# Kernel optimization log

Measured on AMD Instinct MI355X. Metric: run time of the kernel, lower is better.

The kernel has to match this reference:

```python
import jax, jax.numpy as jnp
import numpy as np

N, E, G = 20000, 320000, 128
H, TE, CD = 128, 128, 64
HEADS, DH = 4, 32          # inner = 128 == H
L = 6


def _fwd(p, edge_index, batch):
    """Faithful forward of CrystalDiffusionModel (eval mode: dropout = identity).
    EquivariantGraphConv (imported in the original) is implemented as the standard
    edge-conditioned message-passing conv: m_ij = silu(W[h_src; h_dst; e_ij] + b),
    agg = scatter_add over dst, h' = W_u[h; agg] + b_u."""
    x, ea, t = p['x'], p['edge_attr'], p['t']
    n = x.shape[0]
    h = x @ p['Wn'] + p['bn']                      # [N,H] node embedding
    ef = ea @ p['We'] + p['be']                    # [E,H] edge embedding

    # sinusoidal time embedding -> MLP
    half = TE // 2
    freq = jnp.exp(-jnp.arange(half, dtype=jnp.float32) * (np.log(10000.0) / (half - 1)))
    te = t[:, None] * freq[None, :]
    te = jnp.concatenate([jnp.sin(te), jnp.cos(te)], axis=-1)          # [G,TE]
    te = jax.nn.silu(te @ p['tm_W1'] + p['tm_b1']) @ p['tm_W2'] + p['tm_b2']

    def mlp2(z, W1, b1, W2, b2):
        return jax.nn.silu(z @ W1 + b1) @ W2 + b2

    topo_e = mlp2(p['topo_cond'], p['topo_W1'], p['topo_b1'], p['topo_W2'], p['topo_b2'])
    stab_e = mlp2(p['stab_cond'], p['stab_W1'], p['stab_b1'], p['stab_W2'], p['stab_b2'])
    sust_e = mlp2(p['sust_cond'], p['sust_W1'], p['sust_b1'], p['sust_W2'], p['sust_b2'])
    cond = mlp2(jnp.concatenate([topo_e, stab_e, sust_e], axis=-1),
                p['comb_W1'], p['comb_b1'], p['comb_W2'], p['comb_b2'])  # [G,CD]

    ctx = cond[batch]                               # [N,CD] per-node condition
    # context is a single token per query -> k,v constant across layers
    k = (ctx @ p['Wk']).reshape(n, HEADS, DH)
    v = (ctx @ p['Wv']).reshape(n, HEADS, DH)
    ti = jax.nn.silu(te)[batch]                     # [N,H] time influence (dropout=id)

    src, dst = edge_index[0], edge_index[1]
    scale = DH ** -0.5
    for i in range(L):
        Wm, bm = p['gnn_Wm'][i], p['gnn_bm'][i]
        # split concat-GEMM to avoid materializing [E, 3H]
        m = jax.nn.silu(h[src] @ Wm[:H] + h[dst] @ Wm[H:2 * H] + ef @ Wm[2 * H:] + bm)
        agg = jax.ops.segment_sum(m, dst, num_segments=n)               # [N,H]
        Wu, bu = p['gnn_Wu'][i], p['gnn_bu'][i]
        hu = h @ Wu[:H] + agg @ Wu[H:] + bu
        # LayerNorm
        mu = hu.mean(-1, keepdims=True)
        var = hu.var(-1, keepdims=True)
        hu = (hu - mu) * jax.lax.rsqrt(var + 1e-5) * p['ln_g'][i] + p['ln_b'][i]
        # cross-attention; context length is 1 so softmax over j is exactly 1
        q = (hu @ p['Wq']).reshape(n, HEADS, DH)
        sim = jnp.einsum('nhd,nhd->nh', q, k) * scale                   # [N,heads]
        attn = jax.nn.softmax(sim[..., None], axis=-1)                  # == 1.0
        out = (attn * v).reshape(n, HEADS * DH)
        hu = out @ p['Wo'] + p['bo']
        h = h + hu + ti                              # residual + time influence

    node_pred = jax.nn.silu(h @ p['np_W1'] + p['np_b1']) @ p['np_W2'] + p['np_b2']
    pos_pred = jax.nn.silu(h @ p['pp_W1'] + p['pp_b1']) @ p['pp_W2'] + p['pp_b2']
    return node_pred, pos_pred


def setup_inputs() -> dict:
    key = jax.random.key(0)
    it = iter(jax.random.split(key, 96))

    def nrm(shape, s=0.02):
        return jax.random.normal(next(it), shape, jnp.float32) * s

    z = lambda *s: jnp.zeros(s, jnp.float32)
    inp = {
        'x': jax.random.normal(next(it), (N, 12), jnp.float32),
        'edge_index': jax.random.randint(next(it), (2, E), 0, N),
        'edge_attr': jax.random.normal(next(it), (E, 20), jnp.float32),
        'pos': jax.random.normal(next(it), (N, 3), jnp.float32),
        't': jax.random.uniform(next(it), (G,), jnp.float32) * 1000.0,
        'topo_cond': jax.random.normal(next(it), (G, 7), jnp.float32),
        'stab_cond': jax.random.normal(next(it), (G, 2), jnp.float32),
        'sust_cond': jax.random.normal(next(it), (G, 3), jnp.float32),
        'batch': jnp.sort(jax.random.randint(next(it), (N,), 0, G)),
        'Wn': nrm((12, H)), 'bn': z(H), 'We': nrm((20, H)), 'be': z(H),
        'tm_W1': nrm((TE, 2 * TE)), 'tm_b1': z(2 * TE), 'tm_W2': nrm((2 * TE, TE)), 'tm_b2': z(TE),
        'topo_W1': nrm((7, 32)), 'topo_b1': z(32), 'topo_W2': nrm((32, 32)), 'topo_b2': z(32),
        'stab_W1': nrm((2, 16)), 'stab_b1': z(16), 'stab_W2': nrm((16, 16)), 'stab_b2': z(16),
        'sust_W1': nrm((3, 16)), 'sust_b1': z(16), 'sust_W2': nrm((16, 16)), 'sust_b2': z(16),
        'comb_W1': nrm((64, CD)), 'comb_b1': z(CD), 'comb_W2': nrm((CD, CD)), 'comb_b2': z(CD),
        'Wq': nrm((H, HEADS * DH)), 'Wk': nrm((CD, HEADS * DH)), 'Wv': nrm((CD, HEADS * DH)),
        'Wo': nrm((HEADS * DH, H)), 'bo': z(H),
        'gnn_Wm': nrm((L, 3 * H, H)), 'gnn_bm': z(L, H),
        'gnn_Wu': nrm((L, 2 * H, H)), 'gnn_bu': z(L, H),
        'ln_g': jnp.ones((L, H), jnp.float32), 'ln_b': z(L, H),
        'np_W1': nrm((H, 2 * H)), 'np_b1': z(2 * H), 'np_W2': nrm((2 * H, 12)), 'np_b2': z(12),
        'pp_W1': nrm((H, H)), 'pp_b1': z(H), 'pp_W2': nrm((H, 3)), 'pp_b2': z(3),
    }
    return inp


def reference(x, edge_index, edge_attr, pos, t, topo_cond, stab_cond, sust_cond, batch,
              Wn, bn, We, be, tm_W1, tm_b1, tm_W2, tm_b2,
              topo_W1, topo_b1, topo_W2, topo_b2, stab_W1, stab_b1, stab_W2, stab_b2,
              sust_W1, sust_b1, sust_W2, sust_b2, comb_W1, comb_b1, comb_W2, comb_b2,
              Wq, Wk, Wv, Wo, bo, gnn_Wm, gnn_bm, gnn_Wu, gnn_bu, ln_g, ln_b,
              np_W1, np_b1, np_W2, np_b2, pp_W1, pp_b1, pp_W2, pp_b2):
    loc = dict(locals())
    p = {k: v for k, v in loc.items() if k not in ('edge_index', 'batch', 'pos')}
    return _fwd(p, edge_index, batch)
```

## Files before the change

kernel.cpp:

```cpp
#include <hip/hip_runtime.h>
#include <hip/hip_bf16.h>

#define NN 20000
#define GG 128

typedef __bf16 bf16x8_t __attribute__((ext_vector_type(8)));
typedef float  f32x4_t  __attribute__((ext_vector_type(4)));
typedef __hip_bfloat16 hbf16;

#define PK_NPW1 0
#define PK_PPW1 32768
#define PK_NPW2 49152
#define PK_PPW2 53248
#define PK_WN   55296
#define GADD_OFF 59392

__device__ __forceinline__ float silu_f(float v) {
    return v * __builtin_amdgcn_rcpf(1.0f + __expf(-v));
}

__global__ __launch_bounds__(256) void prep_kernel(
        const float* __restrict__ t, const float* __restrict__ topo,
        const float* __restrict__ stab, const float* __restrict__ sust,
        const float* __restrict__ tmW1, const float* __restrict__ tmb1,
        const float* __restrict__ tmW2, const float* __restrict__ tmb2,
        const float* __restrict__ topoW1, const float* __restrict__ topob1,
        const float* __restrict__ topoW2, const float* __restrict__ topob2,
        const float* __restrict__ stabW1, const float* __restrict__ stabb1,
        const float* __restrict__ stabW2, const float* __restrict__ stabb2,
        const float* __restrict__ sustW1, const float* __restrict__ sustb1,
        const float* __restrict__ sustW2, const float* __restrict__ sustb2,
        const float* __restrict__ combW1, const float* __restrict__ combb1,
        const float* __restrict__ combW2, const float* __restrict__ combb2,
        const float* __restrict__ Wv, const float* __restrict__ Wo,
        const float* __restrict__ bo,
        const float* __restrict__ npW1, const float* __restrict__ npW2,
        const float* __restrict__ ppW1, const float* __restrict__ ppW2,
        const float* __restrict__ Wn,
        float* __restrict__ gadd, hbf16* __restrict__ wsb) {
    const int tid = threadIdx.x;

    if (blockIdx.x >= GG) {
        const int s = (blockIdx.x - GG) * 256 + tid;
        if (s < 32768) {
            const int p = s;
            const int j = p & 7, l = (p >> 3) & 63, kb = (p >> 9) & 3, ct = p >> 11;
            const int k = kb * 32 + ((l >> 4) << 3) + j;
            const int n = ct * 16 + (l & 15);
            wsb[PK_NPW1 + p] = __float2bfloat16(npW1[k * 256 + n]);
        } else if (s < 49152) {
            const int p = s - 32768;
            const int j = p & 7, l = (p >> 3) & 63, kb = (p >> 9) & 3, ct = p >> 11;
            const int k = kb * 32 + ((l >> 4) << 3) + j;
            const int n = ct * 16 + (l & 15);
            wsb[PK_PPW1 + p] = __float2bfloat16(ppW1[k * 128 + n]);
        } else if (s < 53248) {
            const int p = s - 49152;
            const int j = p & 7, l = (p >> 3) & 63, kb = p >> 9;
            const int k = kb * 32 + ((l >> 4) << 3) + j;
            const int n = l & 15;
            wsb[PK_NPW2 + p] = __float2bfloat16(n < 12 ? npW2[k * 12 + n] : 0.0f);
        } else if (s < 55296) {
            const int p = s - 53248;
            const int j = p & 7, l = (p >> 3) & 63, kb = p >> 9;
            const int k = kb * 32 + ((l >> 4) << 3) + j;
            const int n = l & 15;
            wsb[PK_PPW2 + p] = __float2bfloat16(n < 3 ? ppW2[k * 3 + n] : 0.0f);
        } else if (s < 59392) {
            const int p = s - 55296;
            const int j = p & 7, l = (p >> 3) & 63, ct = p >> 9;
            const int k = ((l >> 4) << 3) + j;
            const int n = ct * 16 + (l & 15);
            wsb[PK_WN + p] = __float2bfloat16(k < 12 ? Wn[k * 128 + n] : 0.0f);
        }
        return;
    }

    __shared__ float s_te[128];
    __shared__ float s_th1[256];
    __shared__ float s_tef[128];
    __shared__ float s_l1[64];
    __shared__ float s_cat[64];
    __shared__ float s_c1[64];
    __shared__ float s_cond[64];
    __shared__ float s_v[128];
    __shared__ float s_red[256];

    const int g = blockIdx.x;

    if (tid < 128) {
        const float tval = t[g];
        const int i = tid & 63;
        const float fr = __expf(-(float)i * 0.14619587892025688f);
        const float arg = tval * fr;
        s_te[tid] = (tid < 64) ? sinf(arg) : cosf(arg);
    } else if (tid < 192) {
        const int c = tid - 128;
        if (c < 32) {
            float acc = topob1[c];
            for (int k = 0; k < 7; ++k)
                acc += topo[g * 7 + k] * topoW1[k * 32 + c];
            s_l1[c] = silu_f(acc);
        } else if (c < 48) {
            const int j = c - 32;
            float acc = stabb1[j];
            for (int k = 0; k < 2; ++k)
                acc += stab[g * 2 + k] * stabW1[k * 16 + j];
            s_l1[c] = silu_f(acc);
        } else {
            const int j = c - 48;
            float acc = sustb1[j];
            for (int k = 0; k < 3; ++k)
                acc += sust[g * 3 + k] * sustW1[k * 16 + j];
            s_l1[c] = silu_f(acc);
        }
    }
    __syncthreads();

    {
        float acc = tmb1[tid];
#pragma unroll 16
        for (int k = 0; k < 128; ++k)
            acc += s_te[k] * tmW1[k * 256 + tid];
        s_th1[tid] = silu_f(acc);
    }
    __syncthreads();

    {
        const int j = tid & 127, half = tid >> 7;
        float acc = 0.0f;
#pragma unroll 16
        for (int kk = 0; kk < 128; ++kk)
            acc += s_th1[half * 128 + kk] * tmW2[(half * 128 + kk) * 128 + j];
        s_red[tid] = acc;
    }
    __syncthreads();

    if (tid < 128) {
        s_tef[tid] = tmb2[tid] + s_red[tid] + s_red[tid + 128];
    } else if (tid < 192) {
        const int c = tid - 128;
        if (c < 32) {
            float acc = topob2[c];
            for (int k = 0; k < 32; ++k)
                acc += s_l1[k] * topoW2[k * 32 + c];
            s_cat[c] = acc;
        } else if (c < 48) {
            const int j = c - 32;
            float acc = stabb2[j];
            for (int k = 0; k < 16; ++k)
                acc += s_l1[32 + k] * stabW2[k * 16 + j];
            s_cat[c] = acc;
        } else {
            const int j = c - 48;
            float acc = sustb2[j];
            for (int k = 0; k < 16; ++k)
                acc += s_l1[48 + k] * sustW2[k * 16 + j];
            s_cat[c] = acc;
        }
    }
    __syncthreads();

    {
        const int j = tid & 63, part = tid >> 6;
        float acc = 0.0f;
#pragma unroll
        for (int kk = 0; kk < 16; ++kk)
            acc += s_cat[part * 16 + kk] * combW1[(part * 16 + kk) * 64 + j];
        s_red[tid] = acc;
    }
    __syncthreads();
    if (tid < 64)
        s_c1[tid] = silu_f(combb1[tid] + s_red[tid] + s_red[tid + 64] +
                           s_red[tid + 128] + s_red[tid + 192]);
    __syncthreads();

    {
        const int j = tid & 63, part = tid >> 6;
        float acc = 0.0f;
#pragma unroll
        for (int kk = 0; kk < 16; ++kk)
            acc += s_c1[part * 16 + kk] * combW2[(part * 16 + kk) * 64 + j];
        s_red[tid] = acc;
    }
    __syncthreads();
    if (tid < 64)
        s_cond[tid] = combb2[tid] + s_red[tid] + s_red[tid + 64] +
                      s_red[tid + 128] + s_red[tid + 192];
    __syncthreads();

    {
        const int j = tid & 127, half = tid >> 7;
        float acc = 0.0f;
#pragma unroll 16
        for (int kk = 0; kk < 32; ++kk)
            acc += s_cond[half * 32 + kk] * Wv[(half * 32 + kk) * 128 + j];
        s_red[tid] = acc;
    }
    __syncthreads();
    if (tid < 128) s_v[tid] = s_red[tid] + s_red[tid + 128];
    __syncthreads();

    {
        const int j = tid & 127, half = tid >> 7;
        float acc = 0.0f;
#pragma unroll 16
        for (int kk = 0; kk < 64; ++kk)
            acc += s_v[half * 64 + kk] * Wo[(half * 64 + kk) * 128 + j];
        s_red[tid] = acc;
    }
    __syncthreads();
    if (tid < 128)
        gadd[g * 128 + tid] =
            6.0f * (bo[tid] + s_red[tid] + s_red[tid + 128] + silu_f(s_tef[tid]));
}

#define NGS 8

__global__ __launch_bounds__(256) void node_kernel(
        const float* __restrict__ x, const int* __restrict__ batch,
        const float* __restrict__ bn,
        const float* __restrict__ npb1, const float* __restrict__ npb2,
        const float* __restrict__ ppb1, const float* __restrict__ ppb2,
        const float* __restrict__ gadd, const hbf16* __restrict__ wsb,
        float* __restrict__ out) {
    __shared__ __align__(16) hbf16 s_w[8192];
    __shared__ __align__(16) hbf16 tbuf[4 * 16 * 264];
    __shared__ float s_gadd[NGS * 128];
    __shared__ float s_bias[528];
    __shared__ int   s_bi[64];

    const int tid  = threadIdx.x;
    const int nb   = blockIdx.x * 64;
    const int w    = tid >> 6;
    const int lane = tid & 63;
    const int q    = lane >> 4;
    const int r    = lane & 15;
    const int n16  = nb + w * 16;

    hbf16* wb = tbuf + w * (16 * 264);

    if (tid < 64) {
        int gn = nb + tid;
        if (gn > NN - 1) gn = NN - 1;
        s_bi[tid] = batch[gn];
    }
    {
        int i = tid;
        if (i < 128) s_bias[i] = bn[i];
        else if (i < 384) s_bias[i] = npb1[i - 128];
        else if (i < 396) s_bias[i] = npb2[i - 384];
        else if (i < 524) s_bias[i] = ppb1[i - 396];
        else if (i < 527) s_bias[i] = ppb2[i - 524];
        i = tid + 256;
        if (i < 384) s_bias[i] = npb1[i - 128];
        else if (i < 396) s_bias[i] = npb2[i - 384];
        else if (i < 524) s_bias[i] = ppb1[i - 396];
        else if (i < 527) s_bias[i] = ppb2[i - 524];
    }
    {
        const uint4* src = reinterpret_cast<const uint4*>(wsb + PK_WN);
        uint4* dst = reinterpret_cast<uint4*>(s_w);
        for (int i = tid; i < 512; i += 256) dst[i] = src[i];
    }
    __syncthreads();

    const int g0 = s_bi[0];
    {
        for (int i = tid; i < NGS * 128; i += 256) {
            int gr = g0 + (i >> 7);
            if (gr > GG - 1) gr = GG - 1;
            s_gadd[i] = gadd[gr * 128 + (i & 127)];
        }
    }

    bf16x8_t Ax;
    {
        const int node = n16 + r;
        float xv[8];
#pragma unroll
        for (int j = 0; j < 8; ++j) xv[j] = 0.0f;
        if (node < NN) {
            if (q == 0) {
                const float4 a = *reinterpret_cast<const float4*>(x + node * 12);
                const float4 b = *reinterpret_cast<const float4*>(x + node * 12 + 4);
                xv[0] = a.x; xv[1] = a.y; xv[2] = a.z; xv[3] = a.w;
                xv[4] = b.x; xv[5] = b.y; xv[6] = b.z; xv[7] = b.w;
            } else if (q == 1) {
                const float4 a = *reinterpret_cast<const float4*>(x + node * 12 + 8);
                xv[0] = a.x; xv[1] = a.y; xv[2] = a.z; xv[3] = a.w;
            }
        }
#pragma unroll
        for (int j = 0; j < 8; ++j) {
            const hbf16 tv = __float2bfloat16(xv[j]);
            Ax[j] = *reinterpret_cast<const __bf16*>(&tv);
        }
    }
    __syncthreads();

    {
        f32x4_t hacc[8];
#pragma unroll
        for (int ct = 0; ct < 8; ++ct) {
            const bf16x8_t Bf = *reinterpret_cast<const bf16x8_t*>(
                &s_w[(ct * 64 + lane) * 8]);
            hacc[ct] = __builtin_amdgcn_mfma_f32_16x16x32_bf16(
                Ax, Bf, (f32x4_t){0.f, 0.f, 0.f, 0.f}, 0, 0, 0);
        }
#pragma unroll
        for (int ct = 0; ct < 8; ++ct) {
            const int n = ct * 16 + r;
            const float bv = s_bias[n];
#pragma unroll
            for (int i = 0; i < 4; ++i) {
                const int nl = w * 16 + q * 4 + i;
                const int gi = s_bi[nl] - g0;
                float ga;
                if (gi < NGS) ga = s_gadd[gi * 128 + n];
                else          ga = gadd[(g0 + gi) * 128 + n];
                wb[(q * 4 + i) * 136 + n] = __float2bfloat16(hacc[ct][i] + bv + ga);
            }
        }
    }

    bf16x8_t Ah[4];
#pragma unroll
    for (int kb = 0; kb < 4; ++kb)
        Ah[kb] = *reinterpret_cast<const bf16x8_t*>(
            &wb[r * 136 + kb * 32 + q * 8]);

    for (int c = 0; c < 4; ++c) {
        __syncthreads();
        {
            const uint4* src = reinterpret_cast<const uint4*>(wsb + PK_NPW1 + c * 8192);
            uint4* dst = reinterpret_cast<uint4*>(s_w);
            for (int i = tid; i < 1024; i += 256) dst[i] = src[i];
        }
        __syncthreads();
#pragma unroll
        for (int ci = 0; ci < 4; ++ci) {
            f32x4_t acc = (f32x4_t){0.f, 0.f, 0.f, 0.f};
#pragma unroll
            for (int kb = 0; kb < 4; ++kb) {
                const bf16x8_t Bf = *reinterpret_cast<const bf16x8_t*>(
                    &s_w[((ci * 4 + kb) * 64 + lane) * 8]);
                acc = __builtin_amdgcn_mfma_f32_16x16x32_bf16(Ah[kb], Bf, acc, 0, 0, 0);
            }
            const int ct = c * 4 + ci;
            const int col = ct * 16 + r;
            const float b1 = s_bias[128 + col];
#pragma unroll
            for (int i = 0; i < 4; ++i)
                wb[(q * 4 + i) * 264 + col] = __float2bfloat16(silu_f(acc[i] + b1));
        }
    }

    __syncthreads();
    {
        const uint4* src = reinterpret_cast<const uint4*>(wsb + PK_NPW2);
        uint4* dst = reinterpret_cast<uint4*>(s_w);
        for (int i = tid; i < 512; i += 256) dst[i] = src[i];
    }
    __syncthreads();
    {
        f32x4_t acc2 = (f32x4_t){0.f, 0.f, 0.f, 0.f};
#pragma unroll
        for (int kb = 0; kb < 8; ++kb) {
            const bf16x8_t Af = *reinterpret_cast<const bf16x8_t*>(
                &wb[r * 264 + kb * 32 + q * 8]);
            const bf16x8_t Bf = *reinterpret_cast<const bf16x8_t*>(
                &s_w[(kb * 64 + lane) * 8]);
            acc2 = __builtin_amdgcn_mfma_f32_16x16x32_bf16(Af, Bf, acc2, 0, 0, 0);
        }
        if (r < 12) {
            const float b2 = s_bias[384 + r];
#pragma unroll
            for (int i = 0; i < 4; ++i) {
                const int gn = n16 + q * 4 + i;
                if (gn < NN) out[gn * 12 + r] = acc2[i] + b2;
            }
        }
    }

    for (int c = 0; c < 2; ++c) {
        __syncthreads();
        {
            const uint4* src = reinterpret_cast<const uint4*>(wsb + PK_PPW1 + c * 8192);
            uint4* dst = reinterpret_cast<uint4*>(s_w);
            for (int i = tid; i < 1024; i += 256) dst[i] = src[i];
        }
        __syncthreads();
#pragma unroll
        for (int ci = 0; ci < 4; ++ci) {
            f32x4_t acc = (f32x4_t){0.f, 0.f, 0.f, 0.f};
#pragma unroll
            for (int kb = 0; kb < 4; ++kb) {
                const bf16x8_t Bf = *reinterpret_cast<const bf16x8_t*>(
                    &s_w[((ci * 4 + kb) * 64 + lane) * 8]);
                acc = __builtin_amdgcn_mfma_f32_16x16x32_bf16(Ah[kb], Bf, acc, 0, 0, 0);
            }
            const int ct = c * 4 + ci;
            const int col = ct * 16 + r;
            const float b1 = s_bias[396 + col];
#pragma unroll
            for (int i = 0; i < 4; ++i)
                wb[(q * 4 + i) * 136 + col] = __float2bfloat16(silu_f(acc[i] + b1));
        }
    }

    __syncthreads();
    {
        const uint4* src = reinterpret_cast<const uint4*>(wsb + PK_PPW2);
        uint4* dst = reinterpret_cast<uint4*>(s_w);
        for (int i = tid; i < 256; i += 256) dst[i] = src[i];
    }
    __syncthreads();
    {
        f32x4_t acc2 = (f32x4_t){0.f, 0.f, 0.f, 0.f};
#pragma unroll
        for (int kb = 0; kb < 4; ++kb) {
            const bf16x8_t Af = *reinterpret_cast<const bf16x8_t*>(
                &wb[r * 136 + kb * 32 + q * 8]);
            const bf16x8_t Bf = *reinterpret_cast<const bf16x8_t*>(
                &s_w[(kb * 64 + lane) * 8]);
            acc2 = __builtin_amdgcn_mfma_f32_16x16x32_bf16(Af, Bf, acc2, 0, 0, 0);
        }
        if (r < 3) {
            const float b2 = s_bias[524 + r];
#pragma unroll
            for (int i = 0; i < 4; ++i) {
                const int gn = n16 + q * 4 + i;
                if (gn < NN) out[NN * 12 + gn * 3 + r] = acc2[i] + b2;
            }
        }
    }
}

extern "C" void kernel_launch(void* const* d_in, const int* in_sizes, int n_in,
                              void* d_out, int out_size, void* d_ws, size_t ws_size,
                              hipStream_t stream) {
    const float* x      = (const float*)d_in[0];
    const float* t      = (const float*)d_in[4];
    const float* topo   = (const float*)d_in[5];
    const float* stab   = (const float*)d_in[6];
    const float* sust   = (const float*)d_in[7];
    const int*   batch  = (const int*)d_in[8];
    const float* Wn     = (const float*)d_in[9];
    const float* bn     = (const float*)d_in[10];
    const float* tmW1   = (const float*)d_in[13];
    const float* tmb1   = (const float*)d_in[14];
    const float* tmW2   = (const float*)d_in[15];
    const float* tmb2   = (const float*)d_in[16];
    const float* topoW1 = (const float*)d_in[17];
    const float* topob1 = (const float*)d_in[18];
    const float* topoW2 = (const float*)d_in[19];
    const float* topob2 = (const float*)d_in[20];
    const float* stabW1 = (const float*)d_in[21];
    const float* stabb1 = (const float*)d_in[22];
    const float* stabW2 = (const float*)d_in[23];
    const float* stabb2 = (const float*)d_in[24];
    const float* sustW1 = (const float*)d_in[25];
    const float* sustb1 = (const float*)d_in[26];
    const float* sustW2 = (const float*)d_in[27];
    const float* sustb2 = (const float*)d_in[28];
    const float* combW1 = (const float*)d_in[29];
    const float* combb1 = (const float*)d_in[30];
    const float* combW2 = (const float*)d_in[31];
    const float* combb2 = (const float*)d_in[32];
    const float* Wv     = (const float*)d_in[35];
    const float* Wo     = (const float*)d_in[36];
    const float* bo     = (const float*)d_in[37];
    const float* npW1   = (const float*)d_in[44];
    const float* npb1   = (const float*)d_in[45];
    const float* npW2   = (const float*)d_in[46];
    const float* npb2   = (const float*)d_in[47];
    const float* ppW1   = (const float*)d_in[48];
    const float* ppb1   = (const float*)d_in[49];
    const float* ppW2   = (const float*)d_in[50];
    const float* ppb2   = (const float*)d_in[51];

    hbf16* wsb = (hbf16*)d_ws;
    float* gadd = (float*)(wsb + GADD_OFF);
    float* out = (float*)d_out;

    prep_kernel<<<GG + 232, 256, 0, stream>>>(
        t, topo, stab, sust,
        tmW1, tmb1, tmW2, tmb2,
        topoW1, topob1, topoW2, topob2,
        stabW1, stabb1, stabW2, stabb2,
        sustW1, sustb1, sustW2, sustb2,
        combW1, combb1, combW2, combb2,
        Wv, Wo, bo,
        npW1, npW2, ppW1, ppW2, Wn,
        gadd, wsb);

    node_kernel<<<(NN + 63) / 64, 256, 0, stream>>>(
        x, batch, bn, npb1, npb2, ppb1, ppb2, gadd, wsb, out);
}
```

Baseline: 203.0 us.

## Double-buffer weight tiles with async global-to-LDS loads and widen prep kernel

The node kernel now streams its packed bf16 weight tiles into two alternating LDS buffers using global_load_lds. The next tile's load is issued before the MFMA work on the current tile, so the serialized copy-then-sync phases are replaced by overlapped prefetch. Per-node graph indices are kept in registers instead of a shared array, and NGS drops from 8 to 6. The prep kernel moves to 512 threads with split-K reductions for its small MLPs. Risks include the added LDS footprint lowering occupancy, and the async LDS writes relying on barriers without explicit vmcnt waits.

```diff
diff --git a/kernel.cpp b/kernel.cpp
--- a/kernel.cpp
+++ b/kernel.cpp
@@ -19,7 +19,19 @@
     return v * __builtin_amdgcn_rcpf(1.0f + __expf(-v));
 }
 
-__global__ __launch_bounds__(256) void prep_kernel(
+__device__ __forceinline__ void cp_async(hbf16* dst, const hbf16* src,
+                                         int nbytes, int w, int lane) {
+    const int per_wave = nbytes >> 2;
+    const char* g = (const char*)src + w * per_wave + lane * 16;
+    char* l = (char*)dst + w * per_wave + lane * 16;
+    for (int j = 0; j < per_wave; j += 1024)
+        __builtin_amdgcn_global_load_lds(
+            (__attribute__((address_space(1))) void*)(g + j),
+            (__attribute__((address_space(3))) void*)(l + j),
+            16, 0, 0);
+}
+
+__global__ __launch_bounds__(512) void prep_kernel(
         const float* __restrict__ t, const float* __restrict__ topo,
         const float* __restrict__ stab, const float* __restrict__ sust,
         const float* __restrict__ tmW1, const float* __restrict__ tmb1,
@@ -41,7 +53,7 @@
     const int tid = threadIdx.x;
 
     if (blockIdx.x >= GG) {
-        const int s = (blockIdx.x - GG) * 256 + tid;
+        const int s = (blockIdx.x - GG) * 512 + tid;
         if (s < 32768) {
             const int p = s;
             const int j = p & 7, l = (p >> 3) & 63, kb = (p >> 9) & 3, ct = p >> 11;
@@ -84,7 +96,7 @@
     __shared__ float s_c1[64];
     __shared__ float s_cond[64];
     __shared__ float s_v[128];
-    __shared__ float s_red[256];
+    __shared__ float s_red[512];
 
     const int g = blockIdx.x;
 
@@ -118,26 +130,34 @@
     __syncthreads();
 
     {
-        float acc = tmb1[tid];
-#pragma unroll 16
-        for (int k = 0; k < 128; ++k)
-            acc += s_te[k] * tmW1[k * 256 + tid];
-        s_th1[tid] = silu_f(acc);
-    }
-    __syncthreads();
-
-    {
-        const int j = tid & 127, half = tid >> 7;
+        const int col = tid & 255, half = tid >> 8;
         float acc = 0.0f;
-#pragma unroll 16
-        for (int kk = 0; kk < 128; ++kk)
-            acc += s_th1[half * 128 + kk] * tmW2[(half * 128 + kk) * 128 + j];
-        s_red[tid] = acc;
-    }
-    __syncthreads();
-
+#pragma unroll 32
+        for (int kk = 0; kk < 64; ++kk) {
+            const int k = half * 64 + kk;
+            acc += s_te[k] * tmW1[k * 256 + col];
+        }
+        s_red[half * 256 + col] = acc;
+    }
+    __syncthreads();
+    if (tid < 256)
+        s_th1[tid] = silu_f(tmb1[tid] + s_red[tid] + s_red[256 + tid]);
+    __syncthreads();
+
+    {
+        const int col = tid & 127, qt = tid >> 7;
+        float acc = 0.0f;
+#pragma unroll 32
+        for (int kk = 0; kk < 64; ++kk) {
+            const int k = qt * 64 + kk;
+            acc += s_th1[k] * tmW2[k * 128 + col];
+        }
+        s_red[qt * 128 + col] = acc;
+    }
+    __syncthreads();
     if (tid < 128) {
-        s_tef[tid] = tmb2[tid] + s_red[tid] + s_red[tid + 128];
+        s_tef[tid] = tmb2[tid] + s_red[tid] + s_red[128 + tid] +
+                     s_red[256 + tid] + s_red[384 + tid];
     } else if (tid < 192) {
         const int c = tid - 128;
         if (c < 32) {
@@ -162,60 +182,76 @@
     __syncthreads();
 
     {
-        const int j = tid & 63, part = tid >> 6;
+        const int col = tid & 63, part = tid >> 6;
         float acc = 0.0f;
 #pragma unroll
-        for (int kk = 0; kk < 16; ++kk)
-            acc += s_cat[part * 16 + kk] * combW1[(part * 16 + kk) * 64 + j];
-        s_red[tid] = acc;
-    }
-    __syncthreads();
-    if (tid < 64)
-        s_c1[tid] = silu_f(combb1[tid] + s_red[tid] + s_red[tid + 64] +
-                           s_red[tid + 128] + s_red[tid + 192]);
-    __syncthreads();
-
-    {
-        const int j = tid & 63, part = tid >> 6;
+        for (int kk = 0; kk < 8; ++kk) {
+            const int k = part * 8 + kk;
+            acc += s_cat[k] * combW1[k * 64 + col];
+        }
+        s_red[part * 64 + col] = acc;
+    }
+    __syncthreads();
+    if (tid < 64) {
+        float a = combb1[tid];
+#pragma unroll
+        for (int p = 0; p < 8; ++p) a += s_red[p * 64 + tid];
+        s_c1[tid] = silu_f(a);
+    }
+    __syncthreads();
+
+    {
+        const int col = tid & 63, part = tid >> 6;
         float acc = 0.0f;
 #pragma unroll
-        for (int kk = 0; kk < 16; ++kk)
-            acc += s_c1[part * 16 + kk] * combW2[(part * 16 + kk) * 64 + j];
-        s_red[tid] = acc;
-    }
-    __syncthreads();
-    if (tid < 64)
-        s_cond[tid] = combb2[tid] + s_red[tid] + s_red[tid + 64] +
-                      s_red[tid + 128] + s_red[tid + 192];
-    __syncthreads();
-
-    {
-        const int j = tid & 127, half = tid >> 7;
+        for (int kk = 0; kk < 8; ++kk) {
+            const int k = part * 8 + kk;
+            acc += s_c1[k] * combW2[k * 64 + col];
+        }
+        s_red[part * 64 + col] = acc;
+    }
+    __syncthreads();
+    if (tid < 64) {
+        float a = combb2[tid];
+#pragma unroll
+        for (int p = 0; p < 8; ++p) a += s_red[p * 64 + tid];
+        s_cond[tid] = a;
+    }
+    __syncthreads();
+
+    {
+        const int col = tid & 127, qt = tid >> 7;
         float acc = 0.0f;
-#pragma unroll 16
-        for (int kk = 0; kk < 32; ++kk)
-            acc += s_cond[half * 32 + kk] * Wv[(half * 32 + kk) * 128 + j];
-        s_red[tid] = acc;
-    }
-    __syncthreads();
-    if (tid < 128) s_v[tid] = s_red[tid] + s_red[tid + 128];
-    __syncthreads();
-
-    {
-        const int j = tid & 127, half = tid >> 7;
+#pragma unroll
+        for (int kk = 0; kk < 16; ++kk) {
+            const int k = qt * 16 + kk;
+            acc += s_cond[k] * Wv[k * 128 + col];
+        }
+        s_red[qt * 128 + col] = acc;
+    }
+    __syncthreads();
+    if (tid < 128)
+        s_v[tid] = s_red[tid] + s_red[128 + tid] + s_red[256 + tid] + s_red[384 + tid];
+    __syncthreads();
+
+    {
+        const int col = tid & 127, qt = tid >> 7;
         float acc = 0.0f;
-#pragma unroll 16
-        for (int kk = 0; kk < 64; ++kk)
-            acc += s_v[half * 64 + kk] * Wo[(half * 64 + kk) * 128 + j];
-        s_red[tid] = acc;
+#pragma unroll 32
+        for (int kk = 0; kk < 32; ++kk) {
+            const int k = qt * 32 + kk;
+            acc += s_v[k] * Wo[k * 128 + col];
+        }
+        s_red[qt * 128 + col] = acc;
     }
     __syncthreads();
     if (tid < 128)
-        gadd[g * 128 + tid] =
-            6.0f * (bo[tid] + s_red[tid] + s_red[tid + 128] + silu_f(s_tef[tid]));
+        gadd[g * 128 + tid] = 6.0f * (bo[tid] + s_red[tid] + s_red[128 + tid] +
+                                      s_red[256 + tid] + s_red[384 + tid] +
+                                      silu_f(s_tef[tid]));
 }
 
-#define NGS 8
+#define NGS 6
 
 __global__ __launch_bounds__(256) void node_kernel(
         const float* __restrict__ x, const int* __restrict__ batch,
@@ -224,11 +260,12 @@
         const float* __restrict__ ppb1, const float* __restrict__ ppb2,
         const float* __restrict__ gadd, const hbf16* __restrict__ wsb,
         float* __restrict__ out) {
-    __shared__ __align__(16) hbf16 s_w[8192];
+    __shared__ __align__(16) hbf16 s_wA[8192];
+    __shared__ __align__(16) hbf16 s_wB[8192];
+    __shared__ __align__(16) hbf16 s_wn[4096];
     __shared__ __align__(16) hbf16 tbuf[4 * 16 * 264];
     __shared__ float s_gadd[NGS * 128];
     __shared__ float s_bias[528];
-    __shared__ int   s_bi[64];
 
     const int tid  = threadIdx.x;
     const int nb   = blockIdx.x * 64;
@@ -240,38 +277,24 @@
 
     hbf16* wb = tbuf + w * (16 * 264);
 
-    if (tid < 64) {
-        int gn = nb + tid;
-        if (gn > NN - 1) gn = NN - 1;
-        s_bi[tid] = batch[gn];
-    }
-    {
-        int i = tid;
-        if (i < 128) s_bias[i] = bn[i];
-        else if (i < 384) s_bias[i] = npb1[i - 128];
-        else if (i < 396) s_bias[i] = npb2[i - 384];
-        else if (i < 524) s_bias[i] = ppb1[i - 396];
-        else if (i < 527) s_bias[i] = ppb2[i - 524];
-        i = tid + 256;
-        if (i < 384) s_bias[i] = npb1[i - 128];
-        else if (i < 396) s_bias[i] = npb2[i - 384];
-        else if (i < 524) s_bias[i] = ppb1[i - 396];
-        else if (i < 527) s_bias[i] = ppb2[i - 524];
-    }
-    {
-        const uint4* src = reinterpret_cast<const uint4*>(wsb + PK_WN);
-        uint4* dst = reinterpret_cast<uint4*>(s_w);
-        for (int i = tid; i < 512; i += 256) dst[i] = src[i];
-    }
-    __syncthreads();
-
-    const int g0 = s_bi[0];
-    {
-        for (int i = tid; i < NGS * 128; i += 256) {
-            int gr = g0 + (i >> 7);
-            if (gr > GG - 1) gr = GG - 1;
-            s_gadd[i] = gadd[gr * 128 + (i & 127)];
-        }
+    cp_async(s_wn, wsb + PK_WN, 8192, w, lane);
+    cp_async(s_wA, wsb + PK_NPW1, 16384, w, lane);
+
+    const int g0 = batch[nb];
+    for (int i = tid; i < NGS * 128; i += 256) {
+        int gr = g0 + (i >> 7);
+        if (gr > GG - 1) gr = GG - 1;
+        s_gadd[i] = gadd[gr * 128 + (i & 127)];
+    }
+    for (int i = tid; i < 528; i += 256) {
+        float v;
+        if (i < 128) v = bn[i];
+        else if (i < 384) v = npb1[i - 128];
+        else if (i < 396) v = npb2[i - 384];
+        else if (i < 524) v = ppb1[i - 396];
+        else if (i < 527) v = ppb2[i - 524];
+        else v = 0.0f;
+        s_bias[i] = v;
     }
 
     bf16x8_t Ax;
@@ -297,14 +320,22 @@
             Ax[j] = *reinterpret_cast<const __bf16*>(&tv);
         }
     }
-    __syncthreads();
-
+    int gidx[4];
+#pragma unroll
+    for (int i = 0; i < 4; ++i) {
+        int gn = n16 + q * 4 + i;
+        if (gn > NN - 1) gn = NN - 1;
+        gidx[i] = batch[gn] - g0;
+    }
+    __syncthreads();
+
+    bf16x8_t Ah[4];
     {
         f32x4_t hacc[8];
 #pragma unroll
         for (int ct = 0; ct < 8; ++ct) {
             const bf16x8_t Bf = *reinterpret_cast<const bf16x8_t*>(
-                &s_w[(ct * 64 + lane) * 8]);
+                &s_wn[(ct * 64 + lane) * 8]);
             hacc[ct] = __builtin_amdgcn_mfma_f32_16x16x32_bf16(
                 Ax, Bf, (f32x4_t){0.f, 0.f, 0.f, 0.f}, 0, 0, 0);
         }
@@ -314,55 +345,70 @@
             const float bv = s_bias[n];
 #pragma unroll
             for (int i = 0; i < 4; ++i) {
-                const int nl = w * 16 + q * 4 + i;
-                const int gi = s_bi[nl] - g0;
-                float ga;
-                if (gi < NGS) ga = s_gadd[gi * 128 + n];
-                else          ga = gadd[(g0 + gi) * 128 + n];
+                const int gi = gidx[i];
+                const float ga = (gi < NGS) ? s_gadd[gi * 128 + n]
+                                            : gadd[(g0 + gi) * 128 + n];
                 wb[(q * 4 + i) * 136 + n] = __float2bfloat16(hacc[ct][i] + bv + ga);
             }
         }
-    }
-
-    bf16x8_t Ah[4];
-#pragma unroll
-    for (int kb = 0; kb < 4; ++kb)
-        Ah[kb] = *reinterpret_cast<const bf16x8_t*>(
-            &wb[r * 136 + kb * 32 + q * 8]);
-
-    for (int c = 0; c < 4; ++c) {
-        __syncthreads();
-        {
-            const uint4* src = reinterpret_cast<const uint4*>(wsb + PK_NPW1 + c * 8192);
-            uint4* dst = reinterpret_cast<uint4*>(s_w);
-            for (int i = tid; i < 1024; i += 256) dst[i] = src[i];
-        }
-        __syncthreads();
+#pragma unroll
+        for (int kb = 0; kb < 4; ++kb)
+            Ah[kb] = *reinterpret_cast<const bf16x8_t*>(
+                &wb[r * 136 + kb * 32 + q * 8]);
+    }
+
+    auto npL1_quad = [&](int cbase, const hbf16* sw) {
 #pragma unroll
         for (int ci = 0; ci < 4; ++ci) {
             f32x4_t acc = (f32x4_t){0.f, 0.f, 0.f, 0.f};
 #pragma unroll
             for (int kb = 0; kb < 4; ++kb) {
                 const bf16x8_t Bf = *reinterpret_cast<const bf16x8_t*>(
-                    &s_w[((ci * 4 + kb) * 64 + lane) * 8]);
+                    &sw[((ci * 4 + kb) * 64 + lane) * 8]);
                 acc = __builtin_amdgcn_mfma_f32_16x16x32_bf16(Ah[kb], Bf, acc, 0, 0, 0);
             }
-            const int ct = c * 4 + ci;
-            const int col = ct * 16 + r;
+            const int col = (cbase * 4 + ci) * 16 + r;
             const float b1 = s_bias[128 + col];
 #pragma unroll
             for (int i = 0; i < 4; ++i)
                 wb[(q * 4 + i) * 264 + col] = __float2bfloat16(silu_f(acc[i] + b1));
         }
-    }
-
-    __syncthreads();
-    {
-        const uint4* src = reinterpret_cast<const uint4*>(wsb + PK_NPW2);
-        uint4* dst = reinterpret_cast<uint4*>(s_w);
-        for (int i = tid; i < 512; i += 256) dst[i] = src[i];
-    }
-    __syncthreads();
+    };
+    auto ppL1_quad = [&](int cbase, const hbf16* sw) {
+#pragma unroll
+        for (int ci = 0; ci < 4; ++ci) {
+            f32x4_t acc = (f32x4_t){0.f, 0.f, 0.f, 0.f};
+#pragma unroll
+            for (int kb = 0; kb < 4; ++kb) {
+                const bf16x8_t Bf = *reinterpret_cast<const bf16x8_t*>(
+                    &sw[((ci * 4 + kb) * 64 + lane) * 8]);
+                acc = __builtin_amdgcn_mfma_f32_16x16x32_bf16(Ah[kb], Bf, acc, 0, 0, 0);
+            }
+            const int col = (cbase * 4 + ci) * 16 + r;
+            const float b1 = s_bias[396 + col];
+#pragma unroll
+            for (int i = 0; i < 4; ++i)
+                wb[(q * 4 + i) * 136 + col] = __float2bfloat16(silu_f(acc[i] + b1));
+        }
+    };
+
+    cp_async(s_wB, wsb + PK_NPW1 + 8192, 16384, w, lane);
+    npL1_quad(0, s_wA);
+    __syncthreads();
+
+    cp_async(s_wA, wsb + PK_NPW1 + 16384, 16384, w, lane);
+    npL1_quad(1, s_wB);
+    __syncthreads();
+
+    cp_async(s_wB, wsb + PK_NPW1 + 24576, 16384, w, lane);
+    npL1_quad(2, s_wA);
+    __syncthreads();
+
+    cp_async(s_wA, wsb + PK_NPW2, 8192, w, lane);
+    npL1_quad(3, s_wB);
+    __syncthreads();
+
+    cp_async(s_wB, wsb + PK_PPW1, 16384, w, lane);
     {
         f32x4_t acc2 = (f32x4_t){0.f, 0.f, 0.f, 0.f};
 #pragma unroll
@@ -370,7 +416,7 @@
             const bf16x8_t Af = *reinterpret_cast<const bf16x8_t*>(
                 &wb[r * 264 + kb * 32 + q * 8]);
             const bf16x8_t Bf = *reinterpret_cast<const bf16x8_t*>(
-                &s_w[(kb * 64 + lane) * 8]);
+                &s_wA[(kb * 64 + lane) * 8]);
             acc2 = __builtin_amdgcn_mfma_f32_16x16x32_bf16(Af, Bf, acc2, 0, 0, 0);
         }
         if (r < 12) {
@@ -382,40 +428,16 @@
             }
         }
     }
-
-    for (int c = 0; c < 2; ++c) {
-        __syncthreads();
-        {
-            const uint4* src = reinterpret_cast<const uint4*>(wsb + PK_PPW1 + c * 8192);
-            uint4* dst = reinterpret_cast<uint4*>(s_w);
-            for (int i = tid; i < 1024; i += 256) dst[i] = src[i];
-        }
-        __syncthreads();
-#pragma unroll
-        for (int ci = 0; ci < 4; ++ci) {
-            f32x4_t acc = (f32x4_t){0.f, 0.f, 0.f, 0.f};
-#pragma unroll
-            for (int kb = 0; kb < 4; ++kb) {
-                const bf16x8_t Bf = *reinterpret_cast<const bf16x8_t*>(
-                    &s_w[((ci * 4 + kb) * 64 + lane) * 8]);
-                acc = __builtin_amdgcn_mfma_f32_16x16x32_bf16(Ah[kb], Bf, acc, 0, 0, 0);
-            }
-            const int ct = c * 4 + ci;
-            const int col = ct * 16 + r;
-            const float b1 = s_bias[396 + col];
-#pragma unroll
-            for (int i = 0; i < 4; ++i)
-                wb[(q * 4 + i) * 136 + col] = __float2bfloat16(silu_f(acc[i] + b1));
-        }
-    }
-
-    __syncthreads();
-    {
-        const uint4* src = reinterpret_cast<const uint4*>(wsb + PK_PPW2);
-        uint4* dst = reinterpret_cast<uint4*>(s_w);
-        for (int i = tid; i < 256; i += 256) dst[i] = src[i];
-    }
-    __syncthreads();
+    __syncthreads();
+
+    cp_async(s_wA, wsb + PK_PPW1 + 8192, 16384, w, lane);
+    ppL1_quad(0, s_wB);
+    __syncthreads();
+
+    cp_async(s_wB, wsb + PK_PPW2, 4096, w, lane);
+    ppL1_quad(1, s_wA);
+    __syncthreads();
+
     {
         f32x4_t acc2 = (f32x4_t){0.f, 0.f, 0.f, 0.f};
 #pragma unroll
@@ -423,7 +445,7 @@
             const bf16x8_t Af = *reinterpret_cast<const bf16x8_t*>(
                 &wb[r * 136 + kb * 32 + q * 8]);
             const bf16x8_t Bf = *reinterpret_cast<const bf16x8_t*>(
-                &s_w[(kb * 64 + lane) * 8]);
+                &s_wB[(kb * 64 + lane) * 8]);
             acc2 = __builtin_amdgcn_mfma_f32_16x16x32_bf16(Af, Bf, acc2, 0, 0, 0);
         }
         if (r < 3) {
@@ -484,7 +506,7 @@
     float* gadd = (float*)(wsb + GADD_OFF);
     float* out = (float*)d_out;
 
-    prep_kernel<<<GG + 232, 256, 0, stream>>>(
+    prep_kernel<<<GG + 116, 512, 0, stream>>>(
         t, topo, stab, sust,
         tmW1, tmb1, tmW2, tmb2,
         topoW1, topob1, topoW2, topob2,
```

Result: faster. 194.7 us, median of 2 (-4.1%).
